# Kernel optimization log

Hardware: AMD Instinct MI355X
Metric: run time of the kernel (lower is better)

The kernel has to match this reference:

```python
import jax, jax.numpy as jnp
import numpy as np

N = 50000          # nodes
E = 400000         # edges
MUL0 = 16          # multiplicity of 0e irreps (node & message)
MUL1 = 8           # multiplicity of 1o irreps
RBF = 8
HID = 64
CUTOFF = 5.0
WNUM = MUL0*MUL0 + MUL1*MUL0 + MUL0*MUL1 + MUL1*MUL1  # 576 tp weights per edge
EPS = 1e-8
INV_SQRT3 = 1.0 / np.sqrt(3.0).astype(np.float32)
A_PATH = 1.0 / np.sqrt(float(MUL0 + MUL1))  # e3nn path normalization (fan_in = 24 for both outputs)


def _split_sv(x):
    # x: [n, 40] -> scalars [n,16], vectors [n,8,3]
    return x[:, :MUL0], x[:, MUL0:].reshape(-1, MUL1, 3)


def _irrep_norm(x):
    # RMS-normalize each irrep block separately (IrrepNorm)
    s, v = _split_sv(x)
    s_rms = jnp.sqrt(jnp.mean(s * s, axis=-1, keepdims=True) + EPS)
    v_rms = jnp.sqrt(jnp.mean(jnp.sum(v * v, axis=-1), axis=-1, keepdims=True) + EPS)
    return jnp.concatenate([s / s_rms, (v / v_rms[:, :, None]).reshape(-1, MUL1 * 3)], axis=-1)


def setup_inputs() -> dict:
    key = jax.random.key(0)
    ks = jax.random.split(key, 20)
    inp = {
        'x': jax.random.normal(ks[0], (N, MUL0 + 3 * MUL1), jnp.float32),
        'edge_src': jax.random.randint(ks[1], (E,), 0, N, jnp.int32),
        'edge_dst': jax.random.randint(ks[2], (E,), 0, N, jnp.int32),
        'edge_sh': jax.random.normal(ks[3], (E, 4), jnp.float32),
        'edge_rbf': jax.random.uniform(ks[4], (E, RBF), jnp.float32),
        'edge_len': jax.random.uniform(ks[5], (E,), jnp.float32) * CUTOFF,
        # radial MLP producing per-edge TP weights
        'w_r1': jax.random.normal(ks[6], (RBF, HID), jnp.float32) / np.sqrt(RBF),
        'b_r1': jnp.zeros((HID,), jnp.float32),
        'w_r2': jax.random.normal(ks[7], (HID, WNUM), jnp.float32) / np.sqrt(HID),
        'b_r2': jnp.zeros((WNUM,), jnp.float32),
        # edge gate MLP
        'w_g1': jax.random.normal(ks[8], (RBF, HID), jnp.float32) / np.sqrt(RBF),
        'b_g1': jnp.zeros((HID,), jnp.float32),
        'w_g2': jax.random.normal(ks[9], (HID, 1), jnp.float32) / np.sqrt(HID),
        'b_g2': jnp.zeros((1,), jnp.float32),
        # msg_linear: 16x0e+8x1o -> (16x0e scalars + 8x0e gates) + 8x1o gated
        'Wm_s': jax.random.normal(ks[10], (MUL0, MUL0 + MUL1), jnp.float32),
        'Wm_v': jax.random.normal(ks[11], (MUL1, MUL1), jnp.float32),
        # update_linear and self_linear: 16x0e+8x1o -> 16x0e+8x1o
        'Wu_s': jax.random.normal(ks[12], (MUL0, MUL0), jnp.float32),
        'Wu_v': jax.random.normal(ks[13], (MUL1, MUL1), jnp.float32),
        'Ws_s': jax.random.normal(ks[14], (MUL0, MUL0), jnp.float32),
        'Ws_v': jax.random.normal(ks[15], (MUL1, MUL1), jnp.float32),
        'res_scale': jnp.asarray(0.1, jnp.float32),
    }
    return inp


def reference(x, edge_src, edge_dst, edge_sh, edge_rbf, edge_len,
              w_r1, b_r1, w_r2, b_r2, w_g1, b_g1, w_g2, b_g2,
              Wm_s, Wm_v, Wu_s, Wu_v, Ws_s, Ws_v, res_scale):
    x_norm = _irrep_norm(x)
    xs, xv = _split_sv(x_norm)

    # per-edge TP weights from radial MLP
    w = jax.nn.silu(edge_rbf @ w_r1 + b_r1) @ w_r2 + b_r2            # [E, 576]
    o = MUL0 * MUL0
    w1 = w[:, :o].reshape(-1, MUL0, MUL0)                            # 0e x 0e -> 0e
    w2 = w[:, o:o + MUL1 * MUL0].reshape(-1, MUL1, MUL0)             # 1o x 1o -> 0e
    o += MUL1 * MUL0
    w3 = w[:, o:o + MUL0 * MUL1].reshape(-1, MUL0, MUL1)             # 0e x 1o -> 1o
    o += MUL0 * MUL1
    w4 = w[:, o:].reshape(-1, MUL1, MUL1)                            # 1o x 0e -> 1o

    # gather per-edge source features
    s_e = xs[edge_src]                                               # [E,16]
    v_e = xv[edge_src]                                               # [E,8,3]
    sh0 = edge_sh[:, :1]                                             # [E,1]
    sh1 = edge_sh[:, 1:4]                                            # [E,3]

    # fully-connected tensor product (CG for l<=1, component norm, path norm)
    m0 = A_PATH * (jnp.einsum('ei,eij->ej', s_e * sh0, w1)
                   + INV_SQRT3 * jnp.einsum('eic,ec,eij->ej', v_e, sh1, w2))   # [E,16]
    m1 = A_PATH * (jnp.einsum('ei,eij,ec->ejc', s_e, w3, sh1)
                   + jnp.einsum('eic,eij->ejc', v_e * sh0[:, :, None], w4))    # [E,8,3]

    # cutoff and sigmoid edge gate
    cw = 0.5 * (jnp.cos(jnp.pi * edge_len / CUTOFF) + 1.0) * (edge_len < CUTOFF)
    gw = jax.nn.sigmoid(jax.nn.silu(edge_rbf @ w_g1 + b_g1) @ w_g2 + b_g2)     # [E,1]
    ew = cw[:, None] * gw                                                      # [E,1]
    m0 = m0 * ew
    m1 = m1 * ew[:, :, None]

    # scatter-add into destination nodes, normalize by total edge weight
    agg0 = jax.ops.segment_sum(m0, edge_dst, num_segments=N)                   # [N,16]
    agg1 = jax.ops.segment_sum(m1.reshape(-1, MUL1 * 3), edge_dst, num_segments=N).reshape(-1, MUL1, 3)
    norm = jax.ops.segment_sum(ew, edge_dst, num_segments=N)                   # [N,1]
    norm = jnp.maximum(norm, EPS)
    agg0 = agg0 / norm
    agg1 = agg1 / norm[:, :, None]

    # msg_linear (equivariant linear, fan-in normalized)
    sc = agg0 @ Wm_s / np.sqrt(MUL0)                                           # [N,24]
    vv = jnp.einsum('nic,ij->njc', agg1, Wm_v) / np.sqrt(MUL1)                 # [N,8,3]

    # gated nonlinearity
    scal = jax.nn.silu(sc[:, :MUL0])
    gates = jax.nn.sigmoid(sc[:, MUL0:])
    vg = vv * gates[:, :, None]

    # update + self interaction, residual
    out_s = scal @ Wu_s / np.sqrt(MUL0) + xs @ Ws_s / np.sqrt(MUL0)
    out_v = (jnp.einsum('nic,ij->njc', vg, Wu_v) + jnp.einsum('nic,ij->njc', xv, Ws_v)) / np.sqrt(MUL1)
    out = jnp.concatenate([out_s, out_v.reshape(-1, MUL1 * 3)], axis=-1)
    return x + res_scale * out
```

## Files before the change

kernel.cpp:

```cpp
#include <hip/hip_runtime.h>
#include <cstdint>

#define MUL0 16
#define MUL1 8
#define NRBF 8
#define HID 64
#define WNUM 576
#define CUTOFF 5.0f
#define EPSF 1e-8f

#define INV_SQRT3 0.57735026918962576f
#define A_PATH    0.20412414523193154f
#define Q16       0.25f
#define Q8        0.35355339059327373f
#define PI_OVER_CUT 0.62831853071795865f

typedef _Float16 f16;
typedef _Float16 f16x8 __attribute__((ext_vector_type(8)));
typedef float f32x4 __attribute__((ext_vector_type(4)));

#define MFMA16(a, b, cc) __builtin_amdgcn_mfma_f32_16x16x32_f16(a, b, cc, 0, 0, 0)

__device__ __forceinline__ float sigm(float x) { return 1.0f / (1.0f + __expf(-x)); }

typedef __attribute__((address_space(1))) const unsigned char* gptr_t;
typedef __attribute__((address_space(3))) unsigned char* lptr_t;

__device__ __forceinline__ void stage16(const void* g, void* l) {
  __builtin_amdgcn_global_load_lds((gptr_t)g, (lptr_t)l, 16, 0, 0);
}

extern "C" __global__ __launch_bounds__(256) void k_pre(
    const float* __restrict__ x, float* __restrict__ xnorm,
    float* __restrict__ agg0, float* __restrict__ agg1,
    float* __restrict__ normb, const float* __restrict__ w_r2,
    f16* __restrict__ W2T, const int* __restrict__ edst,
    int* __restrict__ hist, int N, int E) {
  long long gid = (long long)blockIdx.x * 256 + threadIdx.x;

  if (gid < HID * WNUM) {
    int n = (int)gid >> 6, k = (int)gid & 63;
    int jt = n >> 4, cc = n & 15;
    int h = k >> 3, e = k & 7;
    int dst = jt * 1024 + cc * 64 + ((h ^ (cc & 7)) << 3) + e;
    W2T[dst] = (f16)w_r2[k * WNUM + n];
  }

  if (gid < E) atomicAdd(&hist[edst[gid]], 1);

  if (gid < N) {
    long long n = gid;
    const float4* xr = (const float4*)(x + n * 40);
    float4 vv[10];
#pragma unroll
    for (int i = 0; i < 10; i++) vv[i] = xr[i];
    float* f = (float*)vv;
    float ss = 0.f, vs = 0.f;
#pragma unroll
    for (int i = 0; i < 16; i++) ss += f[i] * f[i];
#pragma unroll
    for (int i = 16; i < 40; i++) vs += f[i] * f[i];
    float sr = rsqrtf(ss * (1.0f / 16.0f) + EPSF);
    float vr = rsqrtf(vs * (1.0f / 8.0f) + EPSF);
#pragma unroll
    for (int i = 0; i < 16; i++) f[i] *= sr;
#pragma unroll
    for (int i = 16; i < 40; i++) f[i] *= vr;
    float4* o = (float4*)(xnorm + n * 40);
#pragma unroll
    for (int i = 0; i < 10; i++) o[i] = vv[i];
    float4 z = {0.f, 0.f, 0.f, 0.f};
    float4* pa0 = (float4*)(agg0 + n * 16);
#pragma unroll
    for (int i = 0; i < 4; i++) pa0[i] = z;
    float4* pa1 = (float4*)(agg1 + n * 24);
#pragma unroll
    for (int i = 0; i < 6; i++) pa1[i] = z;
    normb[n] = 0.f;
  }
}

extern "C" __global__ __launch_bounds__(256) void k_scan(
    const int* __restrict__ hist, int* __restrict__ cursor,
    int* __restrict__ pub, int N) {
  __shared__ int sm[256];
  __shared__ int sred[4];
  const int b = blockIdx.x, t = threadIdx.x;
  const int i = b * 256 + t;
  int v = (i < N) ? hist[i] : 0;
  sm[t] = v;
  __syncthreads();
#pragma unroll
  for (int d = 1; d < 256; d <<= 1) {
    int add = (t >= d) ? sm[t - d] : 0;
    __syncthreads();
    sm[t] += add;
    __syncthreads();
  }
  int incl = sm[t];
  if (t == 255)
    __hip_atomic_store(&pub[b], sm[255] + 1, __ATOMIC_RELEASE,
                       __HIP_MEMORY_SCOPE_AGENT);
  int contrib = 0;
  if (t < b) {
    int pv;
    do {
      pv = __hip_atomic_load(&pub[t], __ATOMIC_ACQUIRE,
                             __HIP_MEMORY_SCOPE_AGENT);
    } while (pv == 0);
    contrib = pv - 1;
  }
#pragma unroll
  for (int d = 1; d < 64; d <<= 1) contrib += __shfl_xor(contrib, d);
  __syncthreads();
  if ((t & 63) == 0) sred[t >> 6] = contrib;
  __syncthreads();
  int base = sred[0] + sred[1] + sred[2] + sred[3];
  if (i < N) cursor[i] = base + incl - v;
}

extern "C" __global__ __launch_bounds__(256) void k_scatter(
    const int* __restrict__ edst, int* __restrict__ cursor,
    int* __restrict__ perm, int E) {
  int e = blockIdx.x * 256 + threadIdx.x;
  if (e >= E) return;
  int p = atomicAdd(&cursor[edst[e]], 1);
  perm[p] = e;
}

extern "C" __global__ __launch_bounds__(256, 3) void k_edge(
    const float* __restrict__ xnorm, const int* __restrict__ perm,
    const int* __restrict__ esrc, const int* __restrict__ edst,
    const float* __restrict__ sh, const float* __restrict__ rbf,
    const float* __restrict__ elen,
    const float* __restrict__ w_r1, const float* __restrict__ b_r1,
    const float* __restrict__ w_g1, const float* __restrict__ b_g1,
    const float* __restrict__ w_g2, const float* __restrict__ b_g2,
    const float* __restrict__ b_r2, const f16* __restrict__ W2T,
    float* __restrict__ agg0, float* __restrict__ agg1,
    float* __restrict__ normb, int E) {
  __shared__ __align__(16) char smem[53248];
  f16   (*s_H)[32][72]  = (f16(*)[32][72])(smem);
  float (*s_sn)[32][20] = (float(*)[32][20])(smem + 18432);
  float (*s_v)[32][26]  = (float(*)[32][26])(smem + 28672);
  float (*s_a1)[32][10] = (float(*)[32][10])(smem + 41984);
  float (*s_sh)[32][4]  = (float(*)[32][4])(smem + 47104);
  float (*s_rbf)[32][8] = (float(*)[32][8])(smem + 49152);
  float* s_bias = (float*)(smem + 49152);

  const int t = threadIdx.x;
  const int w = t >> 6;
  const int lane = t & 63;
  const long long eb = (long long)blockIdx.x * 128 + w * 32;

  int pl = 0, dstv = 0, srcv = 0;
  float lenv = 1e9f;
  if (lane < 32) {
    long long g2 = eb + lane;
    if (g2 < E) pl = perm[g2];
    srcv = esrc[pl];
    dstv = edst[pl];
    lenv = elen[pl];
    *(float4*)&s_sh[w][lane][0] = *(const float4*)&sh[(long long)pl * 4];
  }
  {
    int e = lane >> 1, half = lane & 1;
    int pe = __shfl(pl, e);
    *(float4*)&s_rbf[w][e][half * 4] =
        *(const float4*)&rbf[(long long)pe * 8 + half * 4];
  }
  __syncthreads();

  {
    const int ge_l = lane >> 2;
    const int part = lane & 3;
#pragma unroll
    for (int g = 0; g < 2; g++) {
      int e = g * 16 + ge_l;
      int srcn = __shfl(srcv, e);
      const float* xr = xnorm + (long long)srcn * 40;
      if (part < 2) {
        float4 aLo = *(const float4*)(xr + part * 8);
        float4 aHi = *(const float4*)(xr + part * 8 + 4);
        *(float4*)&s_sn[w][e][part * 8] = aLo;
        *(float4*)&s_sn[w][e][part * 8 + 4] = aHi;
      } else {
        const int i0 = (part - 2) * 4;
        const float* vp = xr + 16 + i0 * 3;
        float4 v0 = *(const float4*)(vp);
        float4 v1 = *(const float4*)(vp + 4);
        float4 v2 = *(const float4*)(vp + 8);
        *(float4*)&s_v[w][e][i0 * 3] = v0;
        *(float4*)&s_v[w][e][i0 * 3 + 4] = v1;
        *(float4*)&s_v[w][e][i0 * 3 + 8] = v2;
        float4 shq = *(const float4*)&s_sh[w][e][0];
        float s1x = shq.y, s1y = shq.z, s1z = shq.w;
        s_a1[w][e][i0]     = INV_SQRT3 * (v0.x * s1x + v0.y * s1y + v0.z * s1z);
        s_a1[w][e][i0 + 1] = INV_SQRT3 * (v0.w * s1x + v1.x * s1y + v1.y * s1z);
        s_a1[w][e][i0 + 2] = INV_SQRT3 * (v1.z * s1x + v1.w * s1y + v2.x * s1z);
        s_a1[w][e][i0 + 3] = INV_SQRT3 * (v2.y * s1x + v2.z * s1y + v2.w * s1z);
      }
    }
  }

  {
    float wr[8];
#pragma unroll
    for (int r = 0; r < 8; r++) wr[r] = w_r1[r * HID + lane];
    float bh = b_r1[lane];
#pragma unroll 4
    for (int u = 0; u < 32; u++) {
      float4 ra = *(const float4*)&s_rbf[w][u][0];
      float4 rb2 = *(const float4*)&s_rbf[w][u][4];
      float acc = bh + ra.x * wr[0] + ra.y * wr[1] + ra.z * wr[2] + ra.w * wr[3]
                     + rb2.x * wr[4] + rb2.y * wr[5] + rb2.z * wr[6] + rb2.w * wr[7];
      s_H[w][u][lane] = (f16)(acc * sigm(acc));
    }
  }

  float ewv = 0.f;
  {
    const int eg = lane & 31;
    const int hf = lane >> 5;
    float4 ga = *(const float4*)&s_rbf[w][eg][0];
    float4 gb = *(const float4*)&s_rbf[w][eg][4];
    float rv[8] = {ga.x, ga.y, ga.z, ga.w, gb.x, gb.y, gb.z, gb.w};
    float accp = 0.f;
#pragma unroll
    for (int ch = 0; ch < 2; ch++) {
      const int base = hf * 32 + ch * 16;
      float ttv[16];
      {
        const float4 b0 = *(const float4*)&b_g1[base];
        const float4 b1 = *(const float4*)&b_g1[base + 4];
        const float4 b2 = *(const float4*)&b_g1[base + 8];
        const float4 b3 = *(const float4*)&b_g1[base + 12];
        ttv[0] = b0.x; ttv[1] = b0.y; ttv[2] = b0.z; ttv[3] = b0.w;
        ttv[4] = b1.x; ttv[5] = b1.y; ttv[6] = b1.z; ttv[7] = b1.w;
        ttv[8] = b2.x; ttv[9] = b2.y; ttv[10] = b2.z; ttv[11] = b2.w;
        ttv[12] = b3.x; ttv[13] = b3.y; ttv[14] = b3.z; ttv[15] = b3.w;
      }
#pragma unroll
      for (int r = 0; r < 8; r++) {
        const float* wg = w_g1 + r * HID + base;
        float4 w0 = *(const float4*)(wg);
        float4 w1 = *(const float4*)(wg + 4);
        float4 w2 = *(const float4*)(wg + 8);
        float4 w3 = *(const float4*)(wg + 12);
        float rr = rv[r];
        ttv[0] += rr * w0.x; ttv[1] += rr * w0.y; ttv[2] += rr * w0.z; ttv[3] += rr * w0.w;
        ttv[4] += rr * w1.x; ttv[5] += rr * w1.y; ttv[6] += rr * w1.z; ttv[7] += rr * w1.w;
        ttv[8] += rr * w2.x; ttv[9] += rr * w2.y; ttv[10] += rr * w2.z; ttv[11] += rr * w2.w;
        ttv[12] += rr * w3.x; ttv[13] += rr * w3.y; ttv[14] += rr * w3.z; ttv[15] += rr * w3.w;
      }
      const float4 g0 = *(const float4*)&w_g2[base];
      const float4 g1 = *(const float4*)&w_g2[base + 4];
      const float4 g2 = *(const float4*)&w_g2[base + 8];
      const float4 g3 = *(const float4*)&w_g2[base + 12];
      float gw[16] = {g0.x, g0.y, g0.z, g0.w, g1.x, g1.y, g1.z, g1.w,
                      g2.x, g2.y, g2.z, g2.w, g3.x, g3.y, g3.z, g3.w};
#pragma unroll
      for (int k = 0; k < 16; k++) accp += ttv[k] * sigm(ttv[k]) * gw[k];
    }
    accp += __shfl_xor(accp, 32);
    if (lane < 32) {
      long long g2e = eb + lane;
      if (g2e < E) {
        float cw = (lenv < CUTOFF) ? 0.5f * (__cosf(PI_OVER_CUT * lenv) + 1.0f) : 0.f;
        ewv = cw * sigm(accp + b_g2[0]);
      }
    }
  }
  __syncthreads();

  const int quad = lane >> 4;
  const int c = lane & 15;

  const f16x8 af00 = *(const f16x8*)&s_H[w][c][quad * 8];
  const f16x8 af01 = *(const f16x8*)&s_H[w][c][32 + quad * 8];
  const f16x8 af10 = *(const f16x8*)&s_H[w][16 + c][quad * 8];
  const f16x8 af11 = *(const f16x8*)&s_H[w][16 + c][32 + quad * 8];
  for (int i = t; i < WNUM; i += 256) s_bias[i] = b_r2[i];
  __syncthreads();

  char* ring = smem;
  const char* W2Tc = (const char*)W2T;
  const int lofs = w * 1024;
  const int gofs = w * 1024 + lane * 16;

  stage16(W2Tc + gofs, ring + lofs);
  stage16(W2Tc + 4096 + gofs, ring + 4096 + lofs);

  const int rd0 = c * 128 + ((quad ^ (c & 7)) << 4);
  const int rd1 = c * 128 + (((quad + 4) ^ (c & 7)) << 4);

  float p1[2][4] = {{0.f}}, p2[2][4] = {{0.f}}, t3[2][4] = {{0.f}};
  float mx[2][4] = {{0.f}}, my[2][4] = {{0.f}}, mz[2][4] = {{0.f}};

#pragma unroll 1
  for (int ch = 0; ch < 4; ch++) {
    __syncthreads();
    stage16(W2Tc + (ch + 1) * 8192 + gofs, ring + ((ch + 1) & 1) * 8192 + lofs);
    stage16(W2Tc + (ch + 1) * 8192 + 4096 + gofs,
            ring + ((ch + 1) & 1) * 8192 + 4096 + lofs);
    const char* bb = ring + (ch & 1) * 8192;
#pragma unroll
    for (int q = 0; q < 4; q++) {
      const int jt = ch * 4 + q;
      const char* tb = bb + q * 2048;
      f16x8 b0 = *(const f16x8*)(tb + rd0);
      f16x8 b1 = *(const f16x8*)(tb + rd1);
      float bias = s_bias[jt * 16 + c];
      f32x4 C0 = {0.f, 0.f, 0.f, 0.f};
      C0 = MFMA16(af00, b0, C0); C0 = MFMA16(af01, b1, C0);
      f32x4 C1 = {0.f, 0.f, 0.f, 0.f};
      C1 = MFMA16(af10, b0, C1); C1 = MFMA16(af11, b1, C1);
#pragma unroll
      for (int r = 0; r < 4; r++) {
        p1[0][r] += s_sn[w][quad * 4 + r][jt] * (C0[r] + bias);
        p1[1][r] += s_sn[w][16 + quad * 4 + r][jt] * (C1[r] + bias);
      }
    }
  }
#pragma unroll 1
  for (int ch = 4; ch < 6; ch++) {
    __syncthreads();
    stage16(W2Tc + (ch + 1) * 8192 + gofs, ring + ((ch + 1) & 1) * 8192 + lofs);
    stage16(W2Tc + (ch + 1) * 8192 + 4096 + gofs,
            ring + ((ch + 1) & 1) * 8192 + 4096 + lofs);
    const char* bb = ring + (ch & 1) * 8192;
#pragma unroll
    for (int q = 0; q < 4; q++) {
      const int jt = ch * 4 + q;
      const char* tb = bb + q * 2048;
      f16x8 b0 = *(const f16x8*)(tb + rd0);
      f16x8 b1 = *(const f16x8*)(tb + rd1);
      float bias = s_bias[jt * 16 + c];
      f32x4 C0 = {0.f, 0.f, 0.f, 0.f};
      C0 = MFMA16(af00, b0, C0); C0 = MFMA16(af01, b1, C0);
      f32x4 C1 = {0.f, 0.f, 0.f, 0.f};
      C1 = MFMA16(af10, b0, C1); C1 = MFMA16(af11, b1, C1);
      const int i = jt - 16;
#pragma unroll
      for (int r = 0; r < 4; r++) {
        p2[0][r] += s_a1[w][quad * 4 + r][i] * (C0[r] + bias);
        p2[1][r] += s_a1[w][16 + quad * 4 + r][i] * (C1[r] + bias);
      }
    }
  }
#pragma unroll 1
  for (int ch = 6; ch < 8; ch++) {
    __syncthreads();
    if (ch < 8) {
      stage16(W2Tc + (ch + 1) * 8192 + gofs, ring + ((ch + 1) & 1) * 8192 + lofs);
      stage16(W2Tc + (ch + 1) * 8192 + 4096 + gofs,
              ring + ((ch + 1) & 1) * 8192 + 4096 + lofs);
    }
    const char* bb = ring + (ch & 1) * 8192;
#pragma unroll
    for (int q = 0; q < 4; q++) {
      const int jt = ch * 4 + q;
      const char* tb = bb + q * 2048;
      f16x8 b0 = *(const f16x8*)(tb + rd0);
      f16x8 b1 = *(const f16x8*)(tb + rd1);
      float bias = s_bias[jt * 16 + c];
      f32x4 C0 = {0.f, 0.f, 0.f, 0.f};
      C0 = MFMA16(af00, b0, C0); C0 = MFMA16(af01, b1, C0);
      f32x4 C1 = {0.f, 0.f, 0.f, 0.f};
      C1 = MFMA16(af10, b0, C1); C1 = MFMA16(af11, b1, C1);
      const int i = (jt - 24) * 2 + (c >> 3);
#pragma unroll
      for (int r = 0; r < 4; r++) {
        t3[0][r] += s_sn[w][quad * 4 + r][i] * (C0[r] + bias);
        t3[1][r] += s_sn[w][16 + quad * 4 + r][i] * (C1[r] + bias);
      }
    }
  }
  {
    __syncthreads();
    const char* bb = ring + (8 & 1) * 8192;
#pragma unroll
    for (int q = 0; q < 4; q++) {
      const int jt = 32 + q;
      const char* tb = bb + q * 2048;
      f16x8 b0 = *(const f16x8*)(tb + rd0);
      f16x8 b1 = *(const f16x8*)(tb + rd1);
      float bias = s_bias[jt * 16 + c];
      f32x4 C0 = {0.f, 0.f, 0.f, 0.f};
      C0 = MFMA16(af00, b0, C0); C0 = MFMA16(af01, b1, C0);
      f32x4 C1 = {0.f, 0.f, 0.f, 0.f};
      C1 = MFMA16(af10, b0, C1); C1 = MFMA16(af11, b1, C1);
      const int i = q * 2 + (c >> 3);
#pragma unroll
      for (int r = 0; r < 4; r++) {
        float wv0 = C0[r] + bias;
        float wv1 = C1[r] + bias;
        mx[0][r] += s_v[w][quad * 4 + r][3 * i] * wv0;
        my[0][r] += s_v[w][quad * 4 + r][3 * i + 1] * wv0;
        mz[0][r] += s_v[w][quad * 4 + r][3 * i + 2] * wv0;
        mx[1][r] += s_v[w][16 + quad * 4 + r][3 * i] * wv1;
        my[1][r] += s_v[w][16 + quad * 4 + r][3 * i + 1] * wv1;
        mz[1][r] += s_v[w][16 + quad * 4 + r][3 * i + 2] * wv1;
      }
    }
  }

#pragma unroll
  for (int g = 0; g < 2; g++)
#pragma unroll
    for (int r = 0; r < 4; r++) {
      t3[g][r] += __shfl_xor(t3[g][r], 8);
      mx[g][r] += __shfl_xor(mx[g][r], 8);
      my[g][r] += __shfl_xor(my[g][r], 8);
      mz[g][r] += __shfl_xor(mz[g][r], 8);
    }

#pragma unroll
  for (int g = 0; g < 2; g++) {
    const int e0g = g * 16 + quad * 4;
    int cur = __shfl(dstv, e0g);
    float acc0 = 0.f, a1x = 0.f, a1y = 0.f, a1z = 0.f, nacc = 0.f;
#pragma unroll
    for (int r = 0; r < 4; r++) {
      const int e = e0g + r;
      const int dst = __shfl(dstv, e);
      const float ew = __shfl(ewv, e);
      if (dst != cur) {
        atomicAdd(&agg0[(long long)cur * 16 + c], acc0);
        if (c < 8) {
          long long b = (long long)cur * 24 + (long long)c * 3;
          atomicAdd(&agg1[b], a1x);
          atomicAdd(&agg1[b + 1], a1y);
          atomicAdd(&agg1[b + 2], a1z);
        } else if (c == 8) {
          atomicAdd(&normb[cur], nacc);
        }
        acc0 = a1x = a1y = a1z = nacc = 0.f;
        cur = dst;
      }
      float sc2 = A_PATH * ew;
      float sh0 = s_sh[w][e][0];
      acc0 += (sh0 * p1[g][r] + p2[g][r]) * sc2;
      if (c < 8) {
        float t3v = t3[g][r] * sc2;
        float scs = sc2 * sh0;
        a1x += t3v * s_sh[w][e][1] + mx[g][r] * scs;
        a1y += t3v * s_sh[w][e][2] + my[g][r] * scs;
        a1z += t3v * s_sh[w][e][3] + mz[g][r] * scs;
      } else if (c == 8) {
        nacc += ew;
      }
    }
    atomicAdd(&agg0[(long long)cur * 16 + c], acc0);
    if (c < 8) {
      long long b = (long long)cur * 24 + (long long)c * 3;
      atomicAdd(&agg1[b], a1x);
      atomicAdd(&agg1[b + 1], a1y);
      atomicAdd(&agg1[b + 2], a1z);
    } else if (c == 8) {
      atomicAdd(&normb[cur], nacc);
    }
  }
}

extern "C" __global__ __launch_bounds__(64) void k_node(
    const float* __restrict__ x, const float* __restrict__ xnorm,
    const float* __restrict__ agg0, const float* __restrict__ agg1,
    const float* __restrict__ normb, const float* __restrict__ Wm_s,
    const float* __restrict__ Wm_v, const float* __restrict__ Wu_s,
    const float* __restrict__ Wu_v, const float* __restrict__ Ws_s,
    const float* __restrict__ Ws_v, const float* __restrict__ res_scale_p,
    float* __restrict__ out, int N) {
  __shared__ float sWms[384];
  __shared__ float sWmv[64];
  __shared__ float sWus[256];
  __shared__ float sWuv[64];
  __shared__ float sWss[256];
  __shared__ float sWsv[64];
  int t = threadIdx.x;
  for (int i = t; i < 384; i += 64) sWms[i] = Wm_s[i];
  sWmv[t] = Wm_v[t];
  for (int i = t; i < 256; i += 64) sWus[i] = Wu_s[i];
  sWuv[t] = Wu_v[t];
  for (int i = t; i < 256; i += 64) sWss[i] = Ws_s[i];
  sWsv[t] = Ws_v[t];
  __syncthreads();
  int n = blockIdx.x * 64 + t;
  if (n >= N) return;

  float inv = 1.0f / fmaxf(normb[n], EPSF);
  float4 a04[4], a14[6];
  {
    const float4* p = (const float4*)(agg0 + (long long)n * 16);
#pragma unroll
    for (int i = 0; i < 4; i++) a04[i] = p[i];
    const float4* q = (const float4*)(agg1 + (long long)n * 24);
#pragma unroll
    for (int i = 0; i < 6; i++) a14[i] = q[i];
  }
  float* a0 = (float*)a04;
  float* a1 = (float*)a14;
#pragma unroll
  for (int i = 0; i < 16; i++) a0[i] *= inv;
#pragma unroll
  for (int i = 0; i < 24; i++) a1[i] *= inv;

  float scal[16], gate[8];
#pragma unroll
  for (int jj = 0; jj < 24; jj++) {
    float acc = 0.f;
#pragma unroll
    for (int i = 0; i < 16; i++) acc += a0[i] * sWms[i * 24 + jj];
    acc *= Q16;
    if (jj < 16) scal[jj] = acc * sigm(acc);
    else gate[jj - 16] = sigm(acc);
  }
  float vg[24];
#pragma unroll
  for (int j = 0; j < 8; j++) {
    float g = gate[j];
#pragma unroll
    for (int cc = 0; cc < 3; cc++) {
      float acc = 0.f;
#pragma unroll
      for (int i = 0; i < 8; i++) acc += a1[i * 3 + cc] * sWmv[i * 8 + j];
      vg[j * 3 + cc] = acc * Q8 * g;
    }
  }
  float4 xn4[10], xo4[10];
  {
    const float4* p = (const float4*)(xnorm + (long long)n * 40);
    const float4* q = (const float4*)(x + (long long)n * 40);
#pragma unroll
    for (int i = 0; i < 10; i++) { xn4[i] = p[i]; xo4[i] = q[i]; }
  }
  const float* xn = (const float*)xn4;
  const float* xo = (const float*)xo4;
  float rs = res_scale_p[0];

  float4 ob[10];
  float* ov = (float*)ob;
#pragma unroll
  for (int j = 0; j < 16; j++) {
    float acc = 0.f, acc2 = 0.f;
#pragma unroll
    for (int i = 0; i < 16; i++) {
      acc += scal[i] * sWus[i * 16 + j];
      acc2 += xn[i] * sWss[i * 16 + j];
    }
    ov[j] = xo[j] + rs * ((acc + acc2) * Q16);
  }
#pragma unroll
  for (int j = 0; j < 8; j++) {
#pragma unroll
    for (int cc = 0; cc < 3; cc++) {
      float acc = 0.f;
#pragma unroll
      for (int i = 0; i < 8; i++)
        acc += vg[i * 3 + cc] * sWuv[i * 8 + j] + xn[16 + i * 3 + cc] * sWsv[i * 8 + j];
      ov[16 + j * 3 + cc] = xo[16 + j * 3 + cc] + rs * (acc * Q8);
    }
  }
  float4* po = (float4*)(out + (long long)n * 40);
#pragma unroll
  for (int i = 0; i < 10; i++) po[i] = ob[i];
}

extern "C" void kernel_launch(void* const* d_in, const int* in_sizes, int n_in,
                              void* d_out, int out_size, void* d_ws, size_t ws_size,
                              hipStream_t stream) {
  const float* x = (const float*)d_in[0];
  const int* esrc = (const int*)d_in[1];
  const int* edst = (const int*)d_in[2];
  const float* sh = (const float*)d_in[3];
  const float* rbf = (const float*)d_in[4];
  const float* elen = (const float*)d_in[5];
  const float* w_r1 = (const float*)d_in[6];
  const float* b_r1 = (const float*)d_in[7];
  const float* w_r2 = (const float*)d_in[8];
  const float* b_r2 = (const float*)d_in[9];
  const float* w_g1 = (const float*)d_in[10];
  const float* b_g1 = (const float*)d_in[11];
  const float* w_g2 = (const float*)d_in[12];
  const float* b_g2 = (const float*)d_in[13];
  const float* Wm_s = (const float*)d_in[14];
  const float* Wm_v = (const float*)d_in[15];
  const float* Wu_s = (const float*)d_in[16];
  const float* Wu_v = (const float*)d_in[17];
  const float* Ws_s = (const float*)d_in[18];
  const float* Ws_v = (const float*)d_in[19];
  const float* res_scale = (const float*)d_in[20];

  const int N = in_sizes[0] / 40;
  const int E = in_sizes[1];

  char* ws = (char*)d_ws;
  size_t off = 0;
  float* xnorm = (float*)(ws + off); off += (size_t)N * 40 * sizeof(float);
  off = (off + 255) & ~(size_t)255;
  float* agg0 = (float*)(ws + off); off += (size_t)N * 16 * sizeof(float);
  float* agg1 = (float*)(ws + off); off += (size_t)N * 24 * sizeof(float);
  float* normb = (float*)(ws + off); off += (size_t)N * sizeof(float);
  off = (off + 255) & ~(size_t)255;
  f16* W2T = (f16*)(ws + off); off += (size_t)WNUM * 64 * sizeof(f16);
  off = (off + 255) & ~(size_t)255;
  int* hist   = (int*)(ws + off); off += (size_t)N * sizeof(int);
  int* pub    = (int*)(ws + off); off += 256 * sizeof(int);
  int* cursor = (int*)(ws + off); off += (size_t)N * sizeof(int);
  off = (off + 255) & ~(size_t)255;
  int* perm   = (int*)(ws + off); off += (size_t)E * sizeof(int);

  const int nbE = (E + 255) / 256;
  const int nbN = (N + 255) / 256;

  hipMemsetAsync(hist, 0, ((size_t)N + 256) * sizeof(int), stream);

  k_pre<<<nbE, 256, 0, stream>>>(x, xnorm, agg0, agg1, normb, w_r2, W2T,
                                 edst, hist, N, E);
  k_scan<<<nbN, 256, 0, stream>>>(hist, cursor, pub, N);
  k_scatter<<<nbE, 256, 0, stream>>>(edst, cursor, perm, E);

  int nblk = (E + 127) / 128;
  k_edge<<<nblk, 256, 0, stream>>>(xnorm, perm, esrc, edst, sh, rbf, elen,
                                   w_r1, b_r1, w_g1, b_g1, w_g2, b_g2, b_r2,
                                   W2T, agg0, agg1, normb, E);

  k_node<<<(N + 63) / 64, 64, 0, stream>>>(x, xnorm, agg0, agg1, normb, Wm_s,
                                           Wm_v, Wu_s, Wu_v, Ws_s, Ws_v,
                                           res_scale, (float*)d_out, N);
}
```

Baseline: 339.7 us.

## Drop destination counting sort and process edges in original order

Removes the histogram, prefix-scan and scatter kernels, along with the memset, that built a permutation of edges sorted by destination node. The edge kernel now reads edge attributes directly by edge index, which makes those reads coalesced and saves three launches plus the sort passes. The trade-off is that consecutive edges no longer share a destination. Any warp-level merging of contributions to the same node before the atomic scatter-add is lost, so atomic traffic on the aggregation buffers rises and becomes more random.

```diff
diff --git a/kernel.cpp b/kernel.cpp
--- a/kernel.cpp
+++ b/kernel.cpp
@@ -34,20 +34,17 @@
     const float* __restrict__ x, float* __restrict__ xnorm,
     float* __restrict__ agg0, float* __restrict__ agg1,
     float* __restrict__ normb, const float* __restrict__ w_r2,
-    f16* __restrict__ W2T, const int* __restrict__ edst,
-    int* __restrict__ hist, int N, int E) {
-  long long gid = (long long)blockIdx.x * 256 + threadIdx.x;
+    f16* __restrict__ W2T, int N) {
+  int gid = blockIdx.x * 256 + threadIdx.x;
 
   if (gid < HID * WNUM) {
-    int n = (int)gid >> 6, k = (int)gid & 63;
+    int n = gid >> 6, k = gid & 63;
     int jt = n >> 4, cc = n & 15;
     int h = k >> 3, e = k & 7;
     int dst = jt * 1024 + cc * 64 + ((h ^ (cc & 7)) << 3) + e;
     W2T[dst] = (f16)w_r2[k * WNUM + n];
   }
 
-  if (gid < E) atomicAdd(&hist[edst[gid]], 1);
-
   if (gid < N) {
     long long n = gid;
     const float4* xr = (const float4*)(x + n * 40);
@@ -80,56 +77,8 @@
   }
 }
 
-extern "C" __global__ __launch_bounds__(256) void k_scan(
-    const int* __restrict__ hist, int* __restrict__ cursor,
-    int* __restrict__ pub, int N) {
-  __shared__ int sm[256];
-  __shared__ int sred[4];
-  const int b = blockIdx.x, t = threadIdx.x;
-  const int i = b * 256 + t;
-  int v = (i < N) ? hist[i] : 0;
-  sm[t] = v;
-  __syncthreads();
-#pragma unroll
-  for (int d = 1; d < 256; d <<= 1) {
-    int add = (t >= d) ? sm[t - d] : 0;
-    __syncthreads();
-    sm[t] += add;
-    __syncthreads();
-  }
-  int incl = sm[t];
-  if (t == 255)
-    __hip_atomic_store(&pub[b], sm[255] + 1, __ATOMIC_RELEASE,
-                       __HIP_MEMORY_SCOPE_AGENT);
-  int contrib = 0;
-  if (t < b) {
-    int pv;
-    do {
-      pv = __hip_atomic_load(&pub[t], __ATOMIC_ACQUIRE,
-                             __HIP_MEMORY_SCOPE_AGENT);
-    } while (pv == 0);
-    contrib = pv - 1;
-  }
-#pragma unroll
-  for (int d = 1; d < 64; d <<= 1) contrib += __shfl_xor(contrib, d);
-  __syncthreads();
-  if ((t & 63) == 0) sred[t >> 6] = contrib;
-  __syncthreads();
-  int base = sred[0] + sred[1] + sred[2] + sred[3];
-  if (i < N) cursor[i] = base + incl - v;
-}
-
-extern "C" __global__ __launch_bounds__(256) void k_scatter(
-    const int* __restrict__ edst, int* __restrict__ cursor,
-    int* __restrict__ perm, int E) {
-  int e = blockIdx.x * 256 + threadIdx.x;
-  if (e >= E) return;
-  int p = atomicAdd(&cursor[edst[e]], 1);
-  perm[p] = e;
-}
-
 extern "C" __global__ __launch_bounds__(256, 3) void k_edge(
-    const float* __restrict__ xnorm, const int* __restrict__ perm,
+    const float* __restrict__ xnorm,
     const int* __restrict__ esrc, const int* __restrict__ edst,
     const float* __restrict__ sh, const float* __restrict__ rbf,
     const float* __restrict__ elen,
@@ -153,21 +102,25 @@
   const int lane = t & 63;
   const long long eb = (long long)blockIdx.x * 128 + w * 32;
 
-  int pl = 0, dstv = 0, srcv = 0;
+  int dstv = 0, srcv = 0;
   float lenv = 1e9f;
   if (lane < 32) {
     long long g2 = eb + lane;
-    if (g2 < E) pl = perm[g2];
-    srcv = esrc[pl];
-    dstv = edst[pl];
-    lenv = elen[pl];
-    *(float4*)&s_sh[w][lane][0] = *(const float4*)&sh[(long long)pl * 4];
+    float4 shv = {0.f, 0.f, 0.f, 0.f};
+    if (g2 < E) {
+      srcv = esrc[g2];
+      dstv = edst[g2];
+      lenv = elen[g2];
+      shv = *(const float4*)&sh[g2 * 4];
+    }
+    *(float4*)&s_sh[w][lane][0] = shv;
   }
   {
     int e = lane >> 1, half = lane & 1;
-    int pe = __shfl(pl, e);
-    *(float4*)&s_rbf[w][e][half * 4] =
-        *(const float4*)&rbf[(long long)pe * 8 + half * 4];
+    long long ge2 = eb + e;
+    float4 rv4 = {0.f, 0.f, 0.f, 0.f};
+    if (ge2 < E) rv4 = *(const float4*)&rbf[ge2 * 8 + half * 4];
+    *(float4*)&s_rbf[w][e][half * 4] = rv4;
   }
   __syncthreads();
 
@@ -351,11 +304,9 @@
 #pragma unroll 1
   for (int ch = 6; ch < 8; ch++) {
     __syncthreads();
-    if (ch < 8) {
-      stage16(W2Tc + (ch + 1) * 8192 + gofs, ring + ((ch + 1) & 1) * 8192 + lofs);
-      stage16(W2Tc + (ch + 1) * 8192 + 4096 + gofs,
-              ring + ((ch + 1) & 1) * 8192 + 4096 + lofs);
-    }
+    stage16(W2Tc + (ch + 1) * 8192 + gofs, ring + ((ch + 1) & 1) * 8192 + lofs);
+    stage16(W2Tc + (ch + 1) * 8192 + 4096 + gofs,
+            ring + ((ch + 1) & 1) * 8192 + 4096 + lofs);
     const char* bb = ring + (ch & 1) * 8192;
 #pragma unroll
     for (int q = 0; q < 4; q++) {
@@ -603,25 +554,13 @@
   float* normb = (float*)(ws + off); off += (size_t)N * sizeof(float);
   off = (off + 255) & ~(size_t)255;
   f16* W2T = (f16*)(ws + off); off += (size_t)WNUM * 64 * sizeof(f16);
-  off = (off + 255) & ~(size_t)255;
-  int* hist   = (int*)(ws + off); off += (size_t)N * sizeof(int);
-  int* pub    = (int*)(ws + off); off += 256 * sizeof(int);
-  int* cursor = (int*)(ws + off); off += (size_t)N * sizeof(int);
-  off = (off + 255) & ~(size_t)255;
-  int* perm   = (int*)(ws + off); off += (size_t)E * sizeof(int);
-
-  const int nbE = (E + 255) / 256;
+
   const int nbN = (N + 255) / 256;
 
-  hipMemsetAsync(hist, 0, ((size_t)N + 256) * sizeof(int), stream);
-
-  k_pre<<<nbE, 256, 0, stream>>>(x, xnorm, agg0, agg1, normb, w_r2, W2T,
-                                 edst, hist, N, E);
-  k_scan<<<nbN, 256, 0, stream>>>(hist, cursor, pub, N);
-  k_scatter<<<nbE, 256, 0, stream>>>(edst, cursor, perm, E);
+  k_pre<<<nbN, 256, 0, stream>>>(x, xnorm, agg0, agg1, normb, w_r2, W2T, N);
 
   int nblk = (E + 127) / 128;
-  k_edge<<<nblk, 256, 0, stream>>>(xnorm, perm, esrc, edst, sh, rbf, elen,
+  k_edge<<<nblk, 256, 0, stream>>>(xnorm, esrc, edst, sh, rbf, elen,
                                    w_r1, b_r1, w_g1, b_g1, w_g2, b_g2, b_r2,
                                    W2T, agg0, agg1, normb, E);
 
```

Measured after the change: 329.2 us. 1.03x faster.
